# Performance work log

Measured on AMD Instinct MI355X. Metric: run time of the kernel, lower is better.

Reference implementation:

```python
import jax, jax.numpy as jnp
import numpy as np

P, B, H, W, G, C = 4, 8, 256, 256, 4, 12
N = H * W
PROTO_PER_CLASS = 10


def setup_inputs() -> dict:
    key = jax.random.key(0)
    k1, k2 = jax.random.split(key)
    group_activations = jax.random.normal(k1, (P, B, N, G), dtype=jnp.float32)
    # labels in [0, C]; forward subtracts 1, so 0 becomes the ignored class -1
    target_labels = jax.random.randint(k2, (B, H, W), 0, C + 1)
    # each class owns PROTO_PER_CLASS prototypes (block one-hot) -> sum over col > 0
    proto = np.kron(np.eye(C, dtype=np.float32), np.ones((PROTO_PER_CLASS, 1), np.float32))  # [C*10, C]
    # group_class_identity [P*G, C]: class c assigned to projection (c % P), group (c % G)
    gci = np.zeros((P * G, C), dtype=np.float32)
    for c in range(C):
        gci[(c % P) * G + (c % G), c] = 1.0
    return {
        "group_activations": group_activations,
        "target_labels": target_labels,
        "prototype_class_identity": jnp.asarray(proto),
        "group_class_identity": jnp.asarray(gci),
    }


def reference(group_activations, target_labels, prototype_class_identity, group_class_identity):
    # group_activations: [P, B, N, G] (stacked list_group_activation)
    tl = target_labels.reshape(target_labels.shape[0], -1) - 1           # [B, N], -1 = ignore
    mask = tl[None, :, :] == jnp.arange(C)[:, None, None]                # [C, B, N]
    counts = mask.sum(-1)                                                # [C, B]
    proto_ok = prototype_class_identity.sum(0) > 0                       # [C]
    proj_idx = jnp.argmax(group_class_identity, axis=0) // G             # [C]

    act = group_activations[proj_idx]                                    # [C, B, N, G]
    m4 = mask[..., None]                                                 # [C, B, N, 1]
    neg = jnp.finfo(act.dtype).min
    lse = jax.nn.logsumexp(jnp.where(m4, act, neg), axis=2)              # [C, B, G]
    lse = jnp.where(counts[..., None] > 0, lse, 0.0)                     # avoid inf when empty
    logp = act - lse[:, :, None, :]                                      # masked log_softmax
    lp = jnp.where(m4, logp, 0.0)
    p = jnp.where(m4, jnp.exp(logp), 0.0)

    # T[c,b,a,g] = sum_n p_a * logp_g over masked pixels
    T = jnp.einsum('cbna,cbng->cbag', p, lp)                             # [C, B, G, G]
    diag = jnp.diagonal(T, axis1=-2, axis2=-1)                           # [C, B, G]
    # symmetric KL for pair (j,k): 0.5*(T_kk - T_kj + T_jj - T_jk)
    kld = 0.5 * (diag[..., :, None] + diag[..., None, :] - T - jnp.swapaxes(T, -1, -2))

    pair_mask = jnp.triu(jnp.ones((G, G), bool), 1)                      # j < k
    valid = (counts >= 2) & proto_ok[:, None]                            # [C, B]
    w = valid[..., None, None] & pair_mask                               # [C, B, G, G]
    total = jnp.sum(jnp.where(w, jnp.exp(-kld), 0.0))
    denom = jnp.sum(w)
    return jnp.where(denom > 0, total / denom, jnp.float32(0.0))
```

## Files before the change

kernel.cpp:

```cpp
#include <hip/hip_runtime.h>

#define P_ 4
#define B_ 8
#define NPIX 65536
#define G_ 4
#define C_ 12
#define CHUNKS 64
#define NBLK (B_ * CHUNKS)
#define TILE (NPIX / CHUNKS)
#define ROUNDS (TILE / 64)
#define NSLOT (C_ * B_ * 21)
#define RSTRIDE 65

__global__ __launch_bounds__(256, 2) void kld_stage1(
    const float* __restrict__ act,
    const int*   __restrict__ labels,
    const float* __restrict__ gci,
    float*       __restrict__ partials)
{
    __shared__ float red[4 * 63 * RSTRIDE];
    const int b     = blockIdx.x / CHUNKS;
    const int chunk = blockIdx.x % CHUNKS;
    const int w     = threadIdx.x >> 6;
    const int lane  = threadIdx.x & 63;
    const int cls[3] = { w, w + 4, w + 8 };

    int pj[3];
    #pragma unroll
    for (int k = 0; k < 3; ++k) {
        int best = 0; float bv = gci[cls[k]];
        #pragma unroll
        for (int r = 1; r < P_ * G_; ++r) {
            const float v = gci[r * C_ + cls[k]];
            if (v > bv) { bv = v; best = r; }
        }
        pj[k] = __builtin_amdgcn_readfirstlane(best >> 2);
    }
    const bool same = (pj[1] == pj[0]) && (pj[2] == pj[0]);

    const int* __restrict__ lab = labels + (size_t)b * NPIX + chunk * TILE;
    int lv[ROUNDS];
    #pragma unroll
    for (int r = 0; r < ROUNDS; ++r) lv[r] = lab[r * 64 + lane];

    float acc[63];
    #pragma unroll
    for (int i = 0; i < 63; ++i) acc[i] = 0.0f;

    if (same) {
        const float4* __restrict__ pp = reinterpret_cast<const float4*>(
            act + ((size_t)(pj[0] * B_ + b) * NPIX + (size_t)chunk * TILE) * G_);
        #pragma unroll
        for (int r = 0; r < ROUNDS; ++r) {
            const float4 v = pp[r * 64 + lane];
            const int l   = lv[r];
            const int cef = ((unsigned)(l - 1) < (unsigned)C_) ? (l - 1) : 255;
            const float vv[4] = { v.x, v.y, v.z, v.w };
            float ee[4], wag[16];
            #pragma unroll
            for (int a = 0; a < 4; ++a) ee[a] = __expf(vv[a]);
            #pragma unroll
            for (int a = 0; a < 4; ++a)
                #pragma unroll
                for (int g = 0; g < 4; ++g) wag[a * 4 + g] = ee[a] * vv[g];
            #pragma unroll
            for (int k = 0; k < 3; ++k) {
                const float m = (cef == cls[k]) ? 1.0f : 0.0f;
                acc[k * 21 + 20] += m;
                #pragma unroll
                for (int a = 0; a < 4; ++a)
                    acc[k * 21 + 16 + a] = fmaf(m, ee[a], acc[k * 21 + 16 + a]);
                #pragma unroll
                for (int i = 0; i < 16; ++i)
                    acc[k * 21 + i] = fmaf(m, wag[i], acc[k * 21 + i]);
            }
        }
    } else {
        for (int r = 0; r < ROUNDS; ++r) {
            const int n   = chunk * TILE + r * 64 + lane;
            const int l   = lv[r];
            const int cef = ((unsigned)(l - 1) < (unsigned)C_) ? (l - 1) : 255;
            #pragma unroll
            for (int k = 0; k < 3; ++k) {
                if (cef == cls[k]) {
                    const float4 v = *reinterpret_cast<const float4*>(
                        act + (((size_t)(pj[k] * B_ + b) * NPIX) + (size_t)n) * G_);
                    const float vv[4] = { v.x, v.y, v.z, v.w };
                    #pragma unroll
                    for (int a = 0; a < 4; ++a) {
                        const float e = __expf(vv[a]);
                        acc[k * 21 + 16 + a] += e;
                        #pragma unroll
                        for (int g = 0; g < 4; ++g)
                            acc[k * 21 + a * 4 + g] = fmaf(e, vv[g], acc[k * 21 + a * 4 + g]);
                    }
                    acc[k * 21 + 20] += 1.0f;
                }
            }
        }
    }

    float* base = red + w * 63 * RSTRIDE;
    #pragma unroll
    for (int i = 0; i < 63; ++i) base[i * RSTRIDE + lane] = acc[i];
    __syncthreads();
    if (lane < 63) {
        float s = 0.0f;
        #pragma unroll
        for (int j = 0; j < 64; ++j) s += base[lane * RSTRIDE + j];
        const int k = lane / 21, i = lane % 21;
        const int c = w + k * 4;
        partials[(size_t)chunk * NSLOT + ((size_t)c * B_ + b) * 21 + i] = s;
    }
}

__global__ __launch_bounds__(1024) void kld_finalize(
    const float* __restrict__ partials,
    const float* __restrict__ proto,
    float*       __restrict__ out)
{
    __shared__ float s_sum[NSLOT];
    __shared__ float s_ok[C_];
    __shared__ float s_tot[128];
    __shared__ float s_den[128];
    const int t = threadIdx.x;

    if (t < C_) {
        float s = 0.0f;
        #pragma unroll
        for (int r = 0; r < 120; ++r) s += proto[r * C_ + t];
        s_ok[t] = s;
    }

    for (int s = t; s < NSLOT; s += 1024) {
        float a = 0.0f;
        #pragma unroll
        for (int q = 0; q < CHUNKS; ++q) a += partials[(size_t)q * NSLOT + s];
        s_sum[s] = a;
    }
    __syncthreads();

    float tot = 0.0f, den = 0.0f;
    if (t < C_ * B_) {
        const int c = t / B_;
        const float* slot = s_sum + t * 21;
        const float cnt = slot[20];
        if (s_ok[c] > 0.0f && cnt >= 2.0f) {
            float S[4][4];
            #pragma unroll
            for (int a = 0; a < 4; ++a) {
                const float zinv = 1.0f / slot[16 + a];
                #pragma unroll
                for (int g = 0; g < 4; ++g)
                    S[a][g] = slot[a * 4 + g] * zinv;
            }
            #pragma unroll
            for (int j = 0; j < 4; ++j)
                #pragma unroll
                for (int k = 0; k < 4; ++k)
                    if (k > j) {
                        const float kld = 0.5f * (S[j][j] + S[k][k] - S[j][k] - S[k][j]);
                        tot += __expf(-kld);
                    }
            den = 6.0f;
        }
    }

    if (t < 128) { s_tot[t] = tot; s_den[t] = den; }
    __syncthreads();
    #pragma unroll
    for (int s = 64; s >= 1; s >>= 1) {
        if (t < s) { s_tot[t] += s_tot[t + s]; s_den[t] += s_den[t + s]; }
        __syncthreads();
    }
    if (t == 0)
        out[0] = (s_den[0] > 0.0f) ? (s_tot[0] / s_den[0]) : 0.0f;
}

extern "C" void kernel_launch(void* const* d_in, const int* in_sizes, int n_in,
                              void* d_out, int out_size, void* d_ws, size_t ws_size,
                              hipStream_t stream) {
    const float* act    = (const float*)d_in[0];
    const int*   labels = (const int*)d_in[1];
    const float* proto  = (const float*)d_in[2];
    const float* gci    = (const float*)d_in[3];
    float* out = (float*)d_out;
    float* ws  = (float*)d_ws;

    kld_stage1<<<NBLK, 256, 0, stream>>>(act, labels, gci, ws);
    kld_finalize<<<1, 1024, 0, stream>>>(ws, proto, out);
}
```

Baseline: 87.49 us.

## Fuse finalize into stage1 via fixed-point atomics and last-block reduction

Each block now adds its per-slot partial sums into 64-bit fixed-point global accumulators with atomics, instead of writing per-chunk partials. A completion counter identifies the last block, which reads the totals and computes the final KL score. This removes the separate finalize kernel and its 64-way partial re-read, but adds a memset, many global atomics, and a small quantization of the sums.

```diff
diff --git a/kernel.cpp b/kernel.cpp
--- a/kernel.cpp
+++ b/kernel.cpp
@@ -11,18 +11,28 @@
 #define ROUNDS (TILE / 64)
 #define NSLOT (C_ * B_ * 21)
 #define RSTRIDE 65
+#define SCALE 16777216.0
 
-__global__ __launch_bounds__(256, 2) void kld_stage1(
+__global__ __launch_bounds__(256, 2) void kld_fused(
     const float* __restrict__ act,
     const int*   __restrict__ labels,
     const float* __restrict__ gci,
-    float*       __restrict__ partials)
+    const float* __restrict__ proto,
+    unsigned long long* __restrict__ slots,
+    float* __restrict__ out)
 {
     __shared__ float red[4 * 63 * RSTRIDE];
+    __shared__ float s_sum[NSLOT];
+    __shared__ float s_ok[C_];
+    __shared__ float s_tot[128];
+    __shared__ float s_den[128];
+    __shared__ int   s_last;
+
     const int b     = blockIdx.x / CHUNKS;
     const int chunk = blockIdx.x % CHUNKS;
-    const int w     = threadIdx.x >> 6;
-    const int lane  = threadIdx.x & 63;
+    const int t     = threadIdx.x;
+    const int w     = t >> 6;
+    const int lane  = t & 63;
     const int cls[3] = { w, w + 4, w + 8 };
 
     int pj[3];
@@ -110,33 +120,30 @@
         for (int j = 0; j < 64; ++j) s += base[lane * RSTRIDE + j];
         const int k = lane / 21, i = lane % 21;
         const int c = w + k * 4;
-        partials[(size_t)chunk * NSLOT + ((size_t)c * B_ + b) * 21 + i] = s;
+        const long long q = (long long)((double)s * SCALE);
+        atomicAdd(slots + ((size_t)c * B_ + b) * 21 + i, (unsigned long long)q);
     }
-}
 
-__global__ __launch_bounds__(1024) void kld_finalize(
-    const float* __restrict__ partials,
-    const float* __restrict__ proto,
-    float*       __restrict__ out)
-{
-    __shared__ float s_sum[NSLOT];
-    __shared__ float s_ok[C_];
-    __shared__ float s_tot[128];
-    __shared__ float s_den[128];
-    const int t = threadIdx.x;
+    __threadfence();
+    __syncthreads();
+    unsigned int* counter = (unsigned int*)(slots + NSLOT);
+    if (t == 0) {
+        const unsigned int ret = atomicAdd(counter, 1u);
+        s_last = (ret == (unsigned int)(NBLK - 1)) ? 1 : 0;
+    }
+    __syncthreads();
+    if (!s_last) return;
 
+    const float inv = (float)(1.0 / SCALE);
+    for (int s = t; s < NSLOT; s += 256) {
+        const unsigned long long q = atomicAdd(slots + s, 0ULL);
+        s_sum[s] = (float)((double)(long long)q * (double)inv);
+    }
     if (t < C_) {
         float s = 0.0f;
         #pragma unroll
         for (int r = 0; r < 120; ++r) s += proto[r * C_ + t];
         s_ok[t] = s;
-    }
-
-    for (int s = t; s < NSLOT; s += 1024) {
-        float a = 0.0f;
-        #pragma unroll
-        for (int q = 0; q < CHUNKS; ++q) a += partials[(size_t)q * NSLOT + s];
-        s_sum[s] = a;
     }
     __syncthreads();
 
@@ -185,8 +192,8 @@
     const float* proto  = (const float*)d_in[2];
     const float* gci    = (const float*)d_in[3];
     float* out = (float*)d_out;
-    float* ws  = (float*)d_ws;
+    unsigned long long* slots = (unsigned long long*)d_ws;
 
-    kld_stage1<<<NBLK, 256, 0, stream>>>(act, labels, gci, ws);
-    kld_finalize<<<1, 1024, 0, stream>>>(ws, proto, out);
+    hipMemsetAsync(d_ws, 0, NSLOT * 8 + 64, stream);
+    kld_fused<<<NBLK, 256, 0, stream>>>(act, labels, gci, proto, slots, out);
 }
```

Result: slower. 127.6 us (+45.8%).
